# Kernel tuning notes

Hardware: AMD Instinct MI355X
Metric: run time of the kernel (lower is better)

The kernel has to match this reference:

```python
import jax, jax.numpy as jnp
import numpy as np
from jax import lax

B, L = 4, 2500
Y = 8922
VOCAB = 50002  # vocab_size + 2
E = 100        # embed_size
F = 50         # num_filter_maps
K = 9          # kernel_size
PAD = K // 2


def setup_inputs() -> dict:
    key = jax.random.key(0)
    ks = jax.random.split(key, 8)
    x = jax.random.randint(ks[0], (B, L), 0, VOCAB)
    target = jax.random.uniform(ks[1], (B, Y), dtype=jnp.float32)
    embed_table = jax.random.normal(ks[2], (VOCAB, E), dtype=jnp.float32) * 0.1
    embed_table = embed_table.at[0].set(0.0)  # padding_idx=0
    conv_w = jax.random.normal(ks[3], (F, E, K), dtype=jnp.float32) * (1.0 / np.sqrt(E * K))
    conv_b = jax.random.normal(ks[4], (F,), dtype=jnp.float32) * 0.01
    U_w = jax.random.normal(ks[5], (Y, F), dtype=jnp.float32) * (1.0 / np.sqrt(F))
    final_w = jax.random.normal(ks[6], (Y, F), dtype=jnp.float32) * (1.0 / np.sqrt(F))
    final_b = jax.random.normal(ks[7], (Y,), dtype=jnp.float32) * 0.01
    return {"x": x, "target": target, "embed_table": embed_table,
            "conv_w": conv_w, "conv_b": conv_b, "U_w": U_w,
            "final_w": final_w, "final_b": final_b}


def reference(x, target, embed_table, conv_w, conv_b, U_w, final_w, final_b):
    # embedding lookup (padding_idx=0 rows are zero); dropout is eval-mode identity
    e = embed_table[x] * (x != 0)[..., None].astype(embed_table.dtype)  # [B, L, E]
    # conv1d over sequence: input NCH [B, E, L], kernel OIH [F, E, K], 'same' padding
    h = lax.conv_general_dilated(e.transpose(0, 2, 1), conv_w, (1,), [(PAD, PAD)],
                                 dimension_numbers=("NCH", "OIH", "NCH"))
    h = jnp.tanh(h + conv_b[None, :, None]).transpose(0, 2, 1)  # [B, L, F]
    # label-wise attention
    scores = jnp.einsum("yf,blf->byl", U_w, h)      # [B, Y, L]
    alpha = jax.nn.softmax(scores, axis=2)            # [B, Y, L]
    m = jnp.einsum("byl,blf->byf", alpha, h)         # [B, Y, F]
    y = jnp.einsum("yf,byf->by", final_w, m) + final_b  # [B, Y]
    # BCE with logits, mean reduction
    loss = jnp.mean(jnp.maximum(y, 0.0) - y * target + jnp.log1p(jnp.exp(-jnp.abs(y))))
    yhat = jax.nn.sigmoid(y)
    return (yhat, loss, alpha)
```

## Files before the change

kernel.cpp:

```cpp
#include <hip/hip_runtime.h>
#include <hip/hip_bf16.h>
#include <math.h>

#define B_ 4
#define L_ 2500
#define Y_ 8922
#define E_ 100
#define F_ 50
#define K_ 9

typedef __attribute__((ext_vector_type(8))) short bfrag8;
typedef __attribute__((ext_vector_type(4))) float ffrag4;

#define WS_CWT_F  0
#define WS_HB_U16 90000
#define WS_MP_F   295000
#define BYF_      (B_ * Y_ * F_)
#define BY_       (B_ * Y_)
#define WS_DENP_F (WS_MP_F + 4 * BYF_)
#define WS_PART_F (WS_DENP_F + 4 * BY_)
#define NBLK_FINAL 140

__global__ __launch_bounds__(256) void k0_cwt(const float* __restrict__ conv_w,
                                              float* __restrict__ cwT) {
    int idx = blockIdx.x * 256 + threadIdx.x;
    if (idx < F_ * E_ * K_) {
        int f = idx / (E_ * K_);
        int r = idx % (E_ * K_);
        int e = r / K_;
        int k = r % K_;
        cwT[f * (E_ * K_) + k * E_ + e] = conv_w[idx];
    }
}

#define LT1 32
__global__ __launch_bounds__(256) void k1_embed_conv(
    const int* __restrict__ x, const float* __restrict__ emb_tab,
    const float* __restrict__ cwT, const float* __restrict__ conv_b,
    unsigned short* __restrict__ hb) {
    __shared__ __align__(16) float smem[(LT1 + 8) * E_];
    int b = blockIdx.y;
    int l0 = blockIdx.x * LT1;
    int tid = threadIdx.x;
    for (int idx = tid; idx < (LT1 + 8) * E_; idx += 256) {
        int r = idx / E_, e = idx % E_;
        int l = l0 + r - 4;
        float v = 0.f;
        if (l >= 0 && l < L_) {
            int tok = x[b * L_ + l];
            if (tok != 0) v = emb_tab[tok * E_ + e];
        }
        smem[idx] = v;
    }
    __syncthreads();
    const float4* s4 = (const float4*)smem;
    const float4* w4 = (const float4*)cwT;
    for (int idx = tid; idx < LT1 * F_; idx += 256) {
        int ll = idx / F_, f = idx % F_;
        int l = l0 + ll;
        if (l >= L_) continue;
        float acc = conv_b[f];
        for (int k = 0; k < K_; ++k) {
            const float4* se = s4 + (ll + k) * (E_ / 4);
            const float4* we = w4 + f * (E_ * K_ / 4) + k * (E_ / 4);
#pragma unroll
            for (int e4 = 0; e4 < E_ / 4; ++e4) {
                float4 a = se[e4];
                float4 w = we[e4];
                acc += a.x * w.x + a.y * w.y + a.z * w.z + a.w * w.w;
            }
        }
        __hip_bfloat16 hv = __float2bfloat16(tanhf(acc));
        hb[(size_t)(b * L_ + l) * F_ + f] = *reinterpret_cast<unsigned short*>(&hv);
    }
}

#define YT 64
#define LT 64
#define NLT ((L_ + LT - 1) / LT)
#define NYB ((Y_ + YT - 1) / YT)
#define HSTR 72
#define CH1 4
#define TPC1 (NLT / CH1)
__global__ __launch_bounds__(256) void k2a_denm(
    const float* __restrict__ Uw, const unsigned short* __restrict__ hb,
    float* __restrict__ mp, float* __restrict__ denp) {
    __shared__ unsigned short hlf[64][HSTR];
    __shared__ unsigned short hfl[64][HSTR];
    __shared__ unsigned short psh[4][16][HSTR];

    int b = blockIdx.z;
    int y0 = blockIdx.x * YT;
    int ch = blockIdx.y;
    int tid = threadIdx.x;
    int wv = tid >> 6;
    int lane = tid & 63;
    int col = lane & 15;
    int quad = lane >> 4;
    int ywb = y0 + wv * 16;
    int ym = ywb + col;

    bfrag8 uf[2];
#pragma unroll
    for (int kc = 0; kc < 2; ++kc) {
#pragma unroll
        for (int j = 0; j < 8; ++j) {
            int f = kc * 32 + quad * 8 + j;
            float v = (ym < Y_ && f < F_) ? Uw[(size_t)ym * F_ + f] : 0.f;
            __hip_bfloat16 bv = __float2bfloat16(v);
            uf[kc][j] = *reinterpret_cast<short*>(&bv);
        }
    }

    for (int i = tid; i < 64 * 14; i += 256) {
        int r = i / 14, c = 50 + (i % 14);
        hlf[r][c] = 0;
    }
    for (int i = tid; i < 14 * 64; i += 256) {
        int r = 50 + i / 64, c = i % 64;
        hfl[r][c] = (r == 50) ? (unsigned short)0x3F80 : (unsigned short)0;
    }

    ffrag4 macc[4];
#pragma unroll
    for (int nt = 0; nt < 4; ++nt) macc[nt] = (ffrag4){0.f, 0.f, 0.f, 0.f};

    const unsigned short* hbase = hb + (size_t)b * L_ * F_;

    for (int lt = ch * TPC1; lt < ch * TPC1 + TPC1; ++lt) {
        int l0 = lt * LT;
        __syncthreads();
        const unsigned int* src = (const unsigned int*)(hbase + (size_t)l0 * F_);
        for (int d = tid; d < LT * F_ / 2; d += 256) {
            int r = d / 25, c = d % 25;
            unsigned int v = (l0 + r < L_) ? src[d] : 0u;
            *(unsigned int*)&hlf[r][2 * c] = v;
            hfl[2 * c][r] = (unsigned short)(v & 0xFFFF);
            hfl[2 * c + 1][r] = (unsigned short)(v >> 16);
        }
        __syncthreads();
#pragma unroll
        for (int nt = 0; nt < 4; ++nt) {
            ffrag4 s = (ffrag4){0.f, 0.f, 0.f, 0.f};
#pragma unroll
            for (int kc = 0; kc < 2; ++kc) {
                bfrag8 bf = *(const bfrag8*)&hlf[nt * 16 + col][kc * 32 + quad * 8];
                s = __builtin_amdgcn_mfma_f32_16x16x32_bf16(uf[kc], bf, s, 0, 0, 0);
            }
            int l = l0 + nt * 16 + col;
#pragma unroll
            for (int i = 0; i < 4; ++i) {
                float e = (l < L_) ? __expf(s[i]) : 0.f;
                __hip_bfloat16 be = __float2bfloat16(e);
                psh[wv][quad * 4 + i][nt * 16 + col] = *reinterpret_cast<unsigned short*>(&be);
            }
        }
        __syncthreads();
#pragma unroll
        for (int kc = 0; kc < 2; ++kc) {
            bfrag8 af = *(const bfrag8*)&psh[wv][col][kc * 32 + quad * 8];
#pragma unroll
            for (int nt = 0; nt < 4; ++nt) {
                bfrag8 bf = *(const bfrag8*)&hfl[nt * 16 + col][kc * 32 + quad * 8];
                macc[nt] = __builtin_amdgcn_mfma_f32_16x16x32_bf16(af, bf, macc[nt], 0, 0, 0);
            }
        }
    }

    float* mchunk = mp + (size_t)ch * BYF_;
#pragma unroll
    for (int nt = 0; nt < 4; ++nt) {
        int f = nt * 16 + col;
#pragma unroll
        for (int i = 0; i < 4; ++i) {
            int y = ywb + quad * 4 + i;
            if (y < Y_) {
                if (f < F_) {
                    mchunk[((size_t)b * Y_ + y) * F_ + f] = macc[nt][i];
                } else if (f == F_) {
                    denp[(size_t)ch * BY_ + b * Y_ + y] = macc[nt][i];
                }
            }
        }
    }
}

#define CH2 10
#define TPC2 (NLT / CH2)
__global__ __launch_bounds__(256) void k2b_alpha(
    const float* __restrict__ Uw, const unsigned short* __restrict__ hb,
    const float* __restrict__ denp, float* __restrict__ alpha) {
    __shared__ unsigned short hlf[64][HSTR];
    __shared__ float alf[64][68];

    int b = blockIdx.z;
    int y0 = blockIdx.x * YT;
    int ch = blockIdx.y;
    int tid = threadIdx.x;
    int wv = tid >> 6;
    int lane = tid & 63;
    int col = lane & 15;
    int quad = lane >> 4;
    int ywb = y0 + wv * 16;
    int ym = ywb + col;

    bfrag8 uf[2];
#pragma unroll
    for (int kc = 0; kc < 2; ++kc) {
#pragma unroll
        for (int j = 0; j < 8; ++j) {
            int f = kc * 32 + quad * 8 + j;
            float v = (ym < Y_ && f < F_) ? Uw[(size_t)ym * F_ + f] : 0.f;
            __hip_bfloat16 bv = __float2bfloat16(v);
            uf[kc][j] = *reinterpret_cast<short*>(&bv);
        }
    }

    float rd[4];
#pragma unroll
    for (int i = 0; i < 4; ++i) {
        int y = ywb + quad * 4 + i;
        float d = 0.f;
        if (y < Y_) {
#pragma unroll
            for (int c = 0; c < CH1; ++c) d += denp[(size_t)c * BY_ + b * Y_ + y];
            rd[i] = 1.0f / d;
        } else {
            rd[i] = 0.f;
        }
    }

    for (int i = tid; i < 64 * 14; i += 256) {
        int r = i / 14, c = 50 + (i % 14);
        hlf[r][c] = 0;
    }

    const unsigned short* hbase = hb + (size_t)b * L_ * F_;
    float* aout = alpha + (size_t)b * Y_ * L_;

    for (int lt = ch * TPC2; lt < ch * TPC2 + TPC2; ++lt) {
        int l0 = lt * LT;
        __syncthreads();
        const unsigned int* src = (const unsigned int*)(hbase + (size_t)l0 * F_);
        for (int d = tid; d < LT * F_ / 2; d += 256) {
            int r = d / 25, c = d % 25;
            unsigned int v = (l0 + r < L_) ? src[d] : 0u;
            *(unsigned int*)&hlf[r][2 * c] = v;
        }
        __syncthreads();
#pragma unroll
        for (int nt = 0; nt < 4; ++nt) {
            ffrag4 s = (ffrag4){0.f, 0.f, 0.f, 0.f};
#pragma unroll
            for (int kc = 0; kc < 2; ++kc) {
                bfrag8 bf = *(const bfrag8*)&hlf[nt * 16 + col][kc * 32 + quad * 8];
                s = __builtin_amdgcn_mfma_f32_16x16x32_bf16(uf[kc], bf, s, 0, 0, 0);
            }
            int l = l0 + nt * 16 + col;
#pragma unroll
            for (int i = 0; i < 4; ++i) {
                float v = (l < L_) ? __expf(s[i]) * rd[i] : 0.f;
                alf[wv * 16 + quad * 4 + i][nt * 16 + col] = v;
            }
        }
        __syncthreads();
        int lrem = L_ - l0;
        if (lrem >= LT) {
            for (int i4 = tid; i4 < 64 * 16; i4 += 256) {
                int r = i4 >> 4, c4 = i4 & 15;
                int y = y0 + r;
                if (y < Y_) {
                    float4 v = *(const float4*)&alf[r][c4 * 4];
                    *(float4*)&aout[(size_t)y * L_ + l0 + c4 * 4] = v;
                }
            }
        } else {
            for (int i = tid; i < 64 * LT; i += 256) {
                int r = i >> 6, c = i & 63;
                int y = y0 + r, l = l0 + c;
                if (y < Y_ && l < L_) aout[(size_t)y * L_ + l] = alf[r][c];
            }
        }
    }
}

__global__ __launch_bounds__(256) void k4_final(
    const float* __restrict__ mp, const float* __restrict__ denp,
    const float* __restrict__ fw, const float* __restrict__ fb,
    const float* __restrict__ target, float* __restrict__ yhat,
    float* __restrict__ part) {
    int idx = blockIdx.x * 256 + threadIdx.x;
    float term = 0.f;
    if (idx < B_ * Y_) {
        int yy = idx % Y_;
        const float* wr = fw + (size_t)yy * F_;
        float dot = 0.f;
        float den = 0.f;
#pragma unroll
        for (int c = 0; c < CH1; ++c) {
            den += denp[(size_t)c * BY_ + idx];
            const float* mr = mp + (size_t)c * BYF_ + (size_t)idx * F_;
#pragma unroll
            for (int f = 0; f < F_; ++f) dot += mr[f] * wr[f];
        }
        float s = fb[yy] + dot / den;
        yhat[idx] = 1.f / (1.f + __expf(-s));
        float t = target[idx];
        term = fmaxf(s, 0.f) - s * t + log1pf(__expf(-fabsf(s)));
    }
    float v = term;
    for (int off = 32; off > 0; off >>= 1) v += __shfl_down(v, off, 64);
    __shared__ float red[4];
    int lane = threadIdx.x & 63, w = threadIdx.x >> 6;
    if (lane == 0) red[w] = v;
    __syncthreads();
    if (threadIdx.x == 0) part[blockIdx.x] = red[0] + red[1] + red[2] + red[3];
}

__global__ __launch_bounds__(256) void k5_loss(const float* __restrict__ part,
                                               float* __restrict__ loss_out) {
    float v = 0.f;
    for (int i = threadIdx.x; i < NBLK_FINAL; i += 256) v += part[i];
    for (int off = 32; off > 0; off >>= 1) v += __shfl_down(v, off, 64);
    __shared__ float red[4];
    int lane = threadIdx.x & 63, w = threadIdx.x >> 6;
    if (lane == 0) red[w] = v;
    __syncthreads();
    if (threadIdx.x == 0) loss_out[0] = (red[0] + red[1] + red[2] + red[3]) / (float)(B_ * Y_);
}

extern "C" void kernel_launch(void* const* d_in, const int* in_sizes, int n_in,
                              void* d_out, int out_size, void* d_ws, size_t ws_size,
                              hipStream_t stream) {
    const int*   x       = (const int*)d_in[0];
    const float* target  = (const float*)d_in[1];
    const float* emb_tab = (const float*)d_in[2];
    const float* conv_w  = (const float*)d_in[3];
    const float* conv_b  = (const float*)d_in[4];
    const float* U_w     = (const float*)d_in[5];
    const float* final_w = (const float*)d_in[6];
    const float* final_b = (const float*)d_in[7];

    float* out = (float*)d_out;
    float* wsf = (float*)d_ws;
    unsigned short* wsu = (unsigned short*)d_ws;

    float* cwT            = wsf + WS_CWT_F;
    unsigned short* hbf   = wsu + WS_HB_U16;
    float* mpart          = wsf + WS_MP_F;
    float* denp           = wsf + WS_DENP_F;
    float* part           = wsf + WS_PART_F;

    float* yhat  = out;
    float* loss  = out + (size_t)B_ * Y_;
    float* alpha = loss + 1;

    k0_cwt<<<(F_ * E_ * K_ + 255) / 256, 256, 0, stream>>>(conv_w, cwT);
    k1_embed_conv<<<dim3((L_ + LT1 - 1) / LT1, B_), 256, 0, stream>>>(x, emb_tab, cwT, conv_b, hbf);
    k2a_denm<<<dim3(NYB, CH1, B_), 256, 0, stream>>>(U_w, hbf, mpart, denp);
    k2b_alpha<<<dim3(NYB, CH2, B_), 256, 0, stream>>>(U_w, hbf, denp, alpha);
    k4_final<<<NBLK_FINAL, 256, 0, stream>>>(mpart, denp, final_w, final_b, target, yhat, part);
    k5_loss<<<1, 256, 0, stream>>>(part, loss);
}
```

Before: 832.1 us.

## Precompute transposed h in global memory and drop per-tile LDS transposes and barriers

The conv kernel now writes a second, F-major bf16 copy of h. The denominator/m kernel loads that copy directly into its LDS hfl tile with coalesced 32-bit loads, instead of scattering 16-bit transposed stores per tile. Both attention kernels now stage U_w through LDS with coalesced float2 loads rather than strided per-lane loads. Block-wide barriers between the exp stage and the consumer are replaced with a per-wave lgkmcnt wait, since each wave only reads its own psh/alf rows, and alpha stores become per-wave. The cost is an extra global write and read of h and reliance on wave-private LDS ordering.

```diff
diff --git a/kernel.cpp b/kernel.cpp
--- a/kernel.cpp
+++ b/kernel.cpp
@@ -12,13 +12,15 @@
 typedef __attribute__((ext_vector_type(8))) short bfrag8;
 typedef __attribute__((ext_vector_type(4))) float ffrag4;
 
-#define WS_CWT_F  0
-#define WS_HB_U16 90000
-#define WS_MP_F   295000
-#define BYF_      (B_ * Y_ * F_)
-#define BY_       (B_ * Y_)
-#define WS_DENP_F (WS_MP_F + 4 * BYF_)
-#define WS_PART_F (WS_DENP_F + 4 * BY_)
+#define WS_CWT_F   0
+#define WS_HB_U16  90000
+#define WS_HFL_U16 590000
+#define WS_MP_F    545000
+#define BYF_       (B_ * Y_ * F_)
+#define BY_        (B_ * Y_)
+#define CH1 4
+#define WS_DENP_F  (WS_MP_F + CH1 * BYF_)
+#define WS_PART_F  (WS_DENP_F + CH1 * BY_)
 #define NBLK_FINAL 140
 
 __global__ __launch_bounds__(256) void k0_cwt(const float* __restrict__ conv_w,
@@ -37,7 +39,7 @@
 __global__ __launch_bounds__(256) void k1_embed_conv(
     const int* __restrict__ x, const float* __restrict__ emb_tab,
     const float* __restrict__ cwT, const float* __restrict__ conv_b,
-    unsigned short* __restrict__ hb) {
+    unsigned short* __restrict__ hb, unsigned short* __restrict__ hfl_g) {
     __shared__ __align__(16) float smem[(LT1 + 8) * E_];
     int b = blockIdx.y;
     int l0 = blockIdx.x * LT1;
@@ -71,7 +73,9 @@
             }
         }
         __hip_bfloat16 hv = __float2bfloat16(tanhf(acc));
-        hb[(size_t)(b * L_ + l) * F_ + f] = *reinterpret_cast<unsigned short*>(&hv);
+        unsigned short hu = *reinterpret_cast<unsigned short*>(&hv);
+        hb[(size_t)(b * L_ + l) * F_ + f] = hu;
+        hfl_g[(size_t)b * F_ * L_ + (size_t)f * L_ + l] = hu;
     }
 }
 
@@ -80,14 +84,15 @@
 #define NLT ((L_ + LT - 1) / LT)
 #define NYB ((Y_ + YT - 1) / YT)
 #define HSTR 72
-#define CH1 4
 #define TPC1 (NLT / CH1)
 __global__ __launch_bounds__(256) void k2a_denm(
     const float* __restrict__ Uw, const unsigned short* __restrict__ hb,
+    const unsigned short* __restrict__ hfl_g,
     float* __restrict__ mp, float* __restrict__ denp) {
     __shared__ unsigned short hlf[64][HSTR];
     __shared__ unsigned short hfl[64][HSTR];
     __shared__ unsigned short psh[4][16][HSTR];
+    unsigned short (*ust)[HSTR] = (unsigned short (*)[HSTR])psh;
 
     int b = blockIdx.z;
     int y0 = blockIdx.x * YT;
@@ -98,19 +103,25 @@
     int col = lane & 15;
     int quad = lane >> 4;
     int ywb = y0 + wv * 16;
-    int ym = ywb + col;
-
+
+    for (int d = tid; d < 64 * 25; d += 256) {
+        int r = d / 25, c = d % 25;
+        float2 uv = make_float2(0.f, 0.f);
+        if (y0 + r < Y_) uv = *(const float2*)&Uw[(size_t)(y0 + r) * F_ + 2 * c];
+        __hip_bfloat16 b0 = __float2bfloat16(uv.x);
+        __hip_bfloat16 b1 = __float2bfloat16(uv.y);
+        unsigned int pk = (unsigned int)*reinterpret_cast<unsigned short*>(&b0) |
+                          ((unsigned int)*reinterpret_cast<unsigned short*>(&b1) << 16);
+        *(unsigned int*)&ust[r][2 * c] = pk;
+    }
+    for (int i = tid; i < 64 * 14; i += 256) {
+        int r = i / 14, c = 50 + (i % 14);
+        ust[r][c] = 0;
+    }
+    __syncthreads();
     bfrag8 uf[2];
-#pragma unroll
-    for (int kc = 0; kc < 2; ++kc) {
-#pragma unroll
-        for (int j = 0; j < 8; ++j) {
-            int f = kc * 32 + quad * 8 + j;
-            float v = (ym < Y_ && f < F_) ? Uw[(size_t)ym * F_ + f] : 0.f;
-            __hip_bfloat16 bv = __float2bfloat16(v);
-            uf[kc][j] = *reinterpret_cast<short*>(&bv);
-        }
-    }
+    uf[0] = *(const bfrag8*)&ust[wv * 16 + col][quad * 8];
+    uf[1] = *(const bfrag8*)&ust[wv * 16 + col][32 + quad * 8];
 
     for (int i = tid; i < 64 * 14; i += 256) {
         int r = i / 14, c = 50 + (i % 14);
@@ -125,28 +136,31 @@
 #pragma unroll
     for (int nt = 0; nt < 4; ++nt) macc[nt] = (ffrag4){0.f, 0.f, 0.f, 0.f};
 
-    const unsigned short* hbase = hb + (size_t)b * L_ * F_;
+    const unsigned int* src  = (const unsigned int*)(hb + (size_t)b * L_ * F_);
+    const unsigned int* srcT = (const unsigned int*)(hfl_g + (size_t)b * F_ * L_);
 
     for (int lt = ch * TPC1; lt < ch * TPC1 + TPC1; ++lt) {
         int l0 = lt * LT;
         __syncthreads();
-        const unsigned int* src = (const unsigned int*)(hbase + (size_t)l0 * F_);
         for (int d = tid; d < LT * F_ / 2; d += 256) {
             int r = d / 25, c = d % 25;
-            unsigned int v = (l0 + r < L_) ? src[d] : 0u;
+            unsigned int v = (l0 + r < L_) ? src[l0 * 25 + d] : 0u;
             *(unsigned int*)&hlf[r][2 * c] = v;
-            hfl[2 * c][r] = (unsigned short)(v & 0xFFFF);
-            hfl[2 * c + 1][r] = (unsigned short)(v >> 16);
+        }
+        for (int d = tid; d < LT * F_ / 2; d += 256) {
+            int f = d >> 5, cdw = d & 31;
+            int l = l0 + 2 * cdw;
+            unsigned int v = (l < L_) ? srcT[f * (L_ / 2) + (l0 >> 1) + cdw] : 0u;
+            *(unsigned int*)&hfl[f][2 * cdw] = v;
         }
         __syncthreads();
 #pragma unroll
         for (int nt = 0; nt < 4; ++nt) {
             ffrag4 s = (ffrag4){0.f, 0.f, 0.f, 0.f};
-#pragma unroll
-            for (int kc = 0; kc < 2; ++kc) {
-                bfrag8 bf = *(const bfrag8*)&hlf[nt * 16 + col][kc * 32 + quad * 8];
-                s = __builtin_amdgcn_mfma_f32_16x16x32_bf16(uf[kc], bf, s, 0, 0, 0);
-            }
+            s = __builtin_amdgcn_mfma_f32_16x16x32_bf16(
+                    uf[0], *(const bfrag8*)&hlf[nt * 16 + col][quad * 8], s, 0, 0, 0);
+            s = __builtin_amdgcn_mfma_f32_16x16x32_bf16(
+                    uf[1], *(const bfrag8*)&hlf[nt * 16 + col][32 + quad * 8], s, 0, 0, 0);
             int l = l0 + nt * 16 + col;
 #pragma unroll
             for (int i = 0; i < 4; ++i) {
@@ -155,7 +169,7 @@
                 psh[wv][quad * 4 + i][nt * 16 + col] = *reinterpret_cast<unsigned short*>(&be);
             }
         }
-        __syncthreads();
+        asm volatile("s_waitcnt lgkmcnt(0)" ::: "memory");
 #pragma unroll
         for (int kc = 0; kc < 2; ++kc) {
             bfrag8 af = *(const bfrag8*)&psh[wv][col][kc * 32 + quad * 8];
@@ -191,7 +205,8 @@
     const float* __restrict__ Uw, const unsigned short* __restrict__ hb,
     const float* __restrict__ denp, float* __restrict__ alpha) {
     __shared__ unsigned short hlf[64][HSTR];
-    __shared__ float alf[64][68];
+    __shared__ __align__(16) float alf[64][68];
+    unsigned short (*ust)[HSTR] = (unsigned short (*)[HSTR])alf;
 
     int b = blockIdx.z;
     int y0 = blockIdx.x * YT;
@@ -202,19 +217,25 @@
     int col = lane & 15;
     int quad = lane >> 4;
     int ywb = y0 + wv * 16;
-    int ym = ywb + col;
-
+
+    for (int d = tid; d < 64 * 25; d += 256) {
+        int r = d / 25, c = d % 25;
+        float2 uv = make_float2(0.f, 0.f);
+        if (y0 + r < Y_) uv = *(const float2*)&Uw[(size_t)(y0 + r) * F_ + 2 * c];
+        __hip_bfloat16 b0 = __float2bfloat16(uv.x);
+        __hip_bfloat16 b1 = __float2bfloat16(uv.y);
+        unsigned int pk = (unsigned int)*reinterpret_cast<unsigned short*>(&b0) |
+                          ((unsigned int)*reinterpret_cast<unsigned short*>(&b1) << 16);
+        *(unsigned int*)&ust[r][2 * c] = pk;
+    }
+    for (int i = tid; i < 64 * 14; i += 256) {
+        int r = i / 14, c = 50 + (i % 14);
+        ust[r][c] = 0;
+    }
+    __syncthreads();
     bfrag8 uf[2];
-#pragma unroll
-    for (int kc = 0; kc < 2; ++kc) {
-#pragma unroll
-        for (int j = 0; j < 8; ++j) {
-            int f = kc * 32 + quad * 8 + j;
-            float v = (ym < Y_ && f < F_) ? Uw[(size_t)ym * F_ + f] : 0.f;
-            __hip_bfloat16 bv = __float2bfloat16(v);
-            uf[kc][j] = *reinterpret_cast<short*>(&bv);
-        }
-    }
+    uf[0] = *(const bfrag8*)&ust[wv * 16 + col][quad * 8];
+    uf[1] = *(const bfrag8*)&ust[wv * 16 + col][32 + quad * 8];
 
     float rd[4];
 #pragma unroll
@@ -235,27 +256,25 @@
         hlf[r][c] = 0;
     }
 
-    const unsigned short* hbase = hb + (size_t)b * L_ * F_;
+    const unsigned int* src = (const unsigned int*)(hb + (size_t)b * L_ * F_);
     float* aout = alpha + (size_t)b * Y_ * L_;
 
     for (int lt = ch * TPC2; lt < ch * TPC2 + TPC2; ++lt) {
         int l0 = lt * LT;
         __syncthreads();
-        const unsigned int* src = (const unsigned int*)(hbase + (size_t)l0 * F_);
         for (int d = tid; d < LT * F_ / 2; d += 256) {
             int r = d / 25, c = d % 25;
-            unsigned int v = (l0 + r < L_) ? src[d] : 0u;
+            unsigned int v = (l0 + r < L_) ? src[l0 * 25 + d] : 0u;
             *(unsigned int*)&hlf[r][2 * c] = v;
         }
         __syncthreads();
 #pragma unroll
         for (int nt = 0; nt < 4; ++nt) {
             ffrag4 s = (ffrag4){0.f, 0.f, 0.f, 0.f};
-#pragma unroll
-            for (int kc = 0; kc < 2; ++kc) {
-                bfrag8 bf = *(const bfrag8*)&hlf[nt * 16 + col][kc * 32 + quad * 8];
-                s = __builtin_amdgcn_mfma_f32_16x16x32_bf16(uf[kc], bf, s, 0, 0, 0);
-            }
+            s = __builtin_amdgcn_mfma_f32_16x16x32_bf16(
+                    uf[0], *(const bfrag8*)&hlf[nt * 16 + col][quad * 8], s, 0, 0, 0);
+            s = __builtin_amdgcn_mfma_f32_16x16x32_bf16(
+                    uf[1], *(const bfrag8*)&hlf[nt * 16 + col][32 + quad * 8], s, 0, 0, 0);
             int l = l0 + nt * 16 + col;
 #pragma unroll
             for (int i = 0; i < 4; ++i) {
@@ -263,22 +282,22 @@
                 alf[wv * 16 + quad * 4 + i][nt * 16 + col] = v;
             }
         }
-        __syncthreads();
-        int lrem = L_ - l0;
-        if (lrem >= LT) {
-            for (int i4 = tid; i4 < 64 * 16; i4 += 256) {
-                int r = i4 >> 4, c4 = i4 & 15;
-                int y = y0 + r;
+        asm volatile("s_waitcnt lgkmcnt(0)" ::: "memory");
+        if (l0 + LT <= L_) {
+#pragma unroll
+            for (int it = 0; it < 4; ++it) {
+                int rr = it * 4 + quad;
+                int y = ywb + rr;
                 if (y < Y_) {
-                    float4 v = *(const float4*)&alf[r][c4 * 4];
-                    *(float4*)&aout[(size_t)y * L_ + l0 + c4 * 4] = v;
+                    float4 v = *(const float4*)&alf[wv * 16 + rr][col * 4];
+                    *(float4*)&aout[(size_t)y * L_ + l0 + col * 4] = v;
                 }
             }
         } else {
-            for (int i = tid; i < 64 * LT; i += 256) {
-                int r = i >> 6, c = i & 63;
-                int y = y0 + r, l = l0 + c;
-                if (y < Y_ && l < L_) aout[(size_t)y * L_ + l] = alf[r][c];
+            for (int i = 0; i < 16; ++i) {
+                int y = ywb + i;
+                int l = l0 + lane;
+                if (y < Y_ && l < L_) aout[(size_t)y * L_ + l] = alf[wv * 16 + i][lane];
             }
         }
     }
@@ -347,6 +366,7 @@
 
     float* cwT            = wsf + WS_CWT_F;
     unsigned short* hbf   = wsu + WS_HB_U16;
+    unsigned short* hflg  = wsu + WS_HFL_U16;
     float* mpart          = wsf + WS_MP_F;
     float* denp           = wsf + WS_DENP_F;
     float* part           = wsf + WS_PART_F;
@@ -356,8 +376,9 @@
     float* alpha = loss + 1;
 
     k0_cwt<<<(F_ * E_ * K_ + 255) / 256, 256, 0, stream>>>(conv_w, cwT);
-    k1_embed_conv<<<dim3((L_ + LT1 - 1) / LT1, B_), 256, 0, stream>>>(x, emb_tab, cwT, conv_b, hbf);
-    k2a_denm<<<dim3(NYB, CH1, B_), 256, 0, stream>>>(U_w, hbf, mpart, denp);
+    k1_embed_conv<<<dim3((L_ + LT1 - 1) / LT1, B_), 256, 0, stream>>>(
+        x, emb_tab, cwT, conv_b, hbf, hflg);
+    k2a_denm<<<dim3(NYB, CH1, B_), 256, 0, stream>>>(U_w, hbf, hflg, mpart, denp);
     k2b_alpha<<<dim3(NYB, CH2, B_), 256, 0, stream>>>(U_w, hbf, denp, alpha);
     k4_final<<<NBLK_FINAL, 256, 0, stream>>>(mpart, denp, final_w, final_b, target, yhat, part);
     k5_loss<<<1, 256, 0, stream>>>(part, loss);
```

Result: slower. 850.6 us (+2.2%).
